# Optimization experiments

Hardware: AMD Instinct MI355X
Metric: run time of the kernel (lower is better)

The kernel has to match this reference:

```python
import jax, jax.numpy as jnp
import numpy as np

T, B, I, H, O = 512, 64, 512, 1024, 512


def setup_inputs() -> dict:
    key = jax.random.key(0)
    ks = jax.random.split(key, 12)
    k = 1.0 / np.sqrt(H)  # torch LSTM/Linear init scale
    u = lambda kk, shape: jax.random.uniform(kk, shape, jnp.float32, -k, k)
    return {
        "x": jax.random.normal(ks[0], (T, B, I), jnp.float32),
        # layer 0 (input -> hidden)
        "W_ih0": u(ks[1], (4 * H, I)),
        "W_hh0": u(ks[2], (4 * H, H)),
        "b_ih0": u(ks[3], (4 * H,)),
        "b_hh0": u(ks[4], (4 * H,)),
        # layer 1 (hidden -> hidden)
        "W_ih1": u(ks[5], (4 * H, H)),
        "W_hh1": u(ks[6], (4 * H, H)),
        "b_ih1": u(ks[7], (4 * H,)),
        "b_hh1": u(ks[8], (4 * H,)),
        # output projection
        "W_out": u(ks[9], (O, H)),
        "b_out": u(ks[10], (O,)),
    }


def _lstm_layer(x_seq, W_ih, W_hh, b_ih, b_hh):
    """x_seq: [T, B, in]; returns hidden sequence [T, B, H].
    PyTorch gate order: i, f, g, o."""
    Hh = W_hh.shape[1]
    Bb = x_seq.shape[1]
    # precompute input contribution for all timesteps (one big GEMM)
    pre = jnp.einsum('tbi,gi->tbg', x_seq, W_ih) + b_ih + b_hh  # [T, B, 4H]

    def step(carry, pre_t):
        h, c = carry
        gates = pre_t + h @ W_hh.T  # [B, 4H]
        i, f, g, o = jnp.split(gates, 4, axis=-1)
        i = jax.nn.sigmoid(i)
        f = jax.nn.sigmoid(f)
        g = jnp.tanh(g)
        o = jax.nn.sigmoid(o)
        c = f * c + i * g
        h = o * jnp.tanh(c)
        return (h, c), h

    h0 = jnp.zeros((Bb, Hh), x_seq.dtype)
    c0 = jnp.zeros((Bb, Hh), x_seq.dtype)
    _, hs = jax.lax.scan(step, (h0, c0), pre)
    return hs  # [T, B, H]


def reference(x, W_ih0, W_hh0, b_ih0, b_hh0, W_ih1, W_hh1, b_ih1, b_hh1, W_out, b_out):
    h1 = _lstm_layer(x, W_ih0, W_hh0, b_ih0, b_hh0)   # [T, B, H]
    h2 = _lstm_layer(h1, W_ih1, W_hh1, b_ih1, b_hh1)  # [T, B, H]
    return jnp.einsum('tbh,oh->tbo', h2, W_out) + b_out  # [T, B, O]
```

## Files before the change

### kernel.cpp

```cpp
#include <hip/hip_runtime.h>
#include <hip/hip_bf16.h>
#include <cstdint>
#include <cstddef>

typedef short bf16x8 __attribute__((ext_vector_type(8)));
typedef float f32x4  __attribute__((ext_vector_type(4)));
typedef __hip_bfloat16 bf16;

#define NT_T 512
#define NB   64
#define NI   512
#define NH   1024
#define NO   512

static constexpr size_t SLOT_E = (size_t)NB * NH + 128;
static constexpr size_t SLOT_B = SLOT_E * 2;

static constexpr size_t OFF_XBF   = 0;
static constexpr size_t SZ_XBF    = (size_t)NT_T * NB * NI * 2;
static constexpr size_t OFF_WSW0  = OFF_XBF + SZ_XBF;
static constexpr size_t SZ_WSW0   = 128ull * 98304;
static constexpr size_t OFF_WSW1  = OFF_WSW0 + SZ_WSW0;
static constexpr size_t SZ_WSW1   = 128ull * 131072;
static constexpr size_t OFF_WOUT  = OFF_WSW1 + SZ_WSW1;
static constexpr size_t SZ_WOUT   = (size_t)NO * NH * 2;
static constexpr size_t OFF_B0    = OFF_WOUT + SZ_WOUT;
static constexpr size_t OFF_B1    = OFF_B0 + 4096 * 4;
static constexpr size_t OFF_H1    = OFF_B1 + 4096 * 4;
static constexpr size_t SZ_H1     = (size_t)NT_T * SLOT_B;
static constexpr size_t OFF_H2    = OFF_H1 + SZ_H1;
static constexpr size_t SZ_H2     = (size_t)NT_T * SLOT_B;
static constexpr size_t OFF_FLG   = OFF_H2 + SZ_H2;
static constexpr size_t SZ_FLG    = 2ull * 128 * 512 * 2;

__device__ __forceinline__ float sigm(float x) {
  return 1.0f / (1.0f + __expf(-x));
}
__device__ __forceinline__ float tanh_fast(float x) {
  x = fminf(15.0f, fmaxf(-15.0f, x));
  const float e = __expf(2.0f * x);
  return (e - 1.0f) / (e + 1.0f);
}

__device__ __forceinline__ void waitf1(const unsigned short* f) {
  while (!__all(__hip_atomic_load(f, __ATOMIC_RELAXED, __HIP_MEMORY_SCOPE_AGENT) != 0))
    __builtin_amdgcn_s_sleep(1);
  asm volatile("" ::: "memory");
}
__device__ __forceinline__ void waitf2(const unsigned short* f0, const unsigned short* f1) {
  while (true) {
    const int a = __hip_atomic_load(f0, __ATOMIC_RELAXED, __HIP_MEMORY_SCOPE_AGENT);
    const int b = __hip_atomic_load(f1, __ATOMIC_RELAXED, __HIP_MEMORY_SCOPE_AGENT);
    if (__all((a != 0) && (b != 0))) break;
    __builtin_amdgcn_s_sleep(1);
  }
  asm volatile("" ::: "memory");
}

template <int N>
__device__ __forceinline__ void load_batch(bf16x8 (&A)[N][2], const bf16* p0, const bf16* p1) {
#pragma unroll
  for (int i = 0; i < N; ++i) {
    A[i][0] = *(const bf16x8*)(p0 + i * 32);
    A[i][1] = *(const bf16x8*)(p1 + i * 32);
  }
}

template <int N, int KSW>
__device__ __forceinline__ void mfma_batch(f32x4 (&acc)[2][2], const bf16x8 (&A)[N][2],
                                           const char* Wlds, int ksbase, int lane) {
#pragma unroll
  for (int i = 0; i < N; ++i) {
#pragma unroll
    for (int nt = 0; nt < 2; ++nt) {
      const bf16x8 b = *(const bf16x8*)(Wlds + ((size_t)(nt * KSW + ksbase + i) * 64 + lane) * 16);
      acc[0][nt] = __builtin_amdgcn_mfma_f32_16x16x32_bf16(A[i][0], b, acc[0][nt], 0, 0, 0);
      acc[1][nt] = __builtin_amdgcn_mfma_f32_16x16x32_bf16(A[i][1], b, acc[1][nt], 0, 0, 0);
    }
  }
}

__global__ void k_convert_x(const float* __restrict__ x, bf16* __restrict__ xbf) {
  const size_t n = (size_t)NT_T * NB * NI;
  for (size_t i = (size_t)blockIdx.x * blockDim.x + threadIdx.x; i < n;
       i += (size_t)gridDim.x * blockDim.x)
    xbf[i] = __float2bfloat16(x[i]);
}

__global__ void k_build_wsw(const float* __restrict__ Wih0, const float* __restrict__ Whh0,
                            const float* __restrict__ Wih1, const float* __restrict__ Whh1,
                            bf16* __restrict__ wsw0, bf16* __restrict__ wsw1) {
  const size_t L0N = 128ull * 2 * 48 * 64 * 8;
  const size_t L1N = 128ull * 2 * 64 * 64 * 8;
  const size_t n = L0N + L1N;
  for (size_t i = (size_t)blockIdx.x * blockDim.x + threadIdx.x; i < n;
       i += (size_t)gridDim.x * blockDim.x) {
    if (i < L0N) {
      size_t idx = i;
      const int j = idx & 7;    idx >>= 3;
      const int lane = idx & 63; idx >>= 6;
      const int ks = (int)(idx % 48); idx /= 48;
      const int nt = idx & 1;
      const int blk = (int)(idx >> 1);
      const int nl = nt * 16 + (lane & 15);
      const int k = ks * 32 + (lane >> 4) * 8 + j;
      const int grow = (nl >> 3) * 1024 + blk * 8 + (nl & 7);
      const float v = (k < 512) ? Wih0[(size_t)grow * 512 + k]
                                : Whh0[(size_t)grow * 1024 + (k - 512)];
      wsw0[i] = __float2bfloat16(v);
    } else {
      size_t idx = i - L0N;
      const size_t o = idx;
      const int j = idx & 7;    idx >>= 3;
      const int lane = idx & 63; idx >>= 6;
      const int ks = (int)(idx % 64); idx /= 64;
      const int nt = idx & 1;
      const int blk = (int)(idx >> 1);
      const int nl = nt * 16 + (lane & 15);
      const int k = ks * 32 + (lane >> 4) * 8 + j;
      const int grow = (nl >> 3) * 1024 + blk * 8 + (nl & 7);
      const float v = (k < 1024) ? Wih1[(size_t)grow * 1024 + k]
                                 : Whh1[(size_t)grow * 1024 + (k - 1024)];
      wsw1[o] = __float2bfloat16(v);
    }
  }
}

__global__ void k_small(const float* __restrict__ Wout,
                        const float* __restrict__ bih0, const float* __restrict__ bhh0,
                        const float* __restrict__ bih1, const float* __restrict__ bhh1,
                        bf16* __restrict__ woutbf, float* __restrict__ bias0,
                        float* __restrict__ bias1, unsigned int* __restrict__ flg) {
  const int i = blockIdx.x * 256 + threadIdx.x;
  if (i < NO * NH) woutbf[i] = __float2bfloat16(Wout[i]);
  if (i < 4096) {
    bias0[i] = bih0[i] + bhh0[i];
    bias1[i] = bih1[i] + bhh1[i];
  }
  if (i < (int)(SZ_FLG / 4)) flg[i] = 0u;
}

__global__ __launch_bounds__(256, 1) void lstm_recur(
    const bf16* __restrict__ xbf, const bf16* __restrict__ wsw0, const bf16* __restrict__ wsw1,
    const float* __restrict__ bias0, const float* __restrict__ bias1,
    bf16* __restrict__ h1hist, bf16* __restrict__ h2hist, unsigned short* __restrict__ flg) {
  __shared__ char Wlds[131072];
  __shared__ float red[64][33];

  const int tid = threadIdx.x;
  const int bid = blockIdx.x;
  const int layer = bid >> 7;
  const int blk = bid & 127;
  const int lane = tid & 63;
  const int wid = tid >> 6;
  const int mh = wid & 1;
  const int kh = wid >> 1;
  const int q = lane >> 4;
  const int ml = lane & 15;
  const int colbase = blk * 8;
  const int row0 = mh * 32 + ml;
  const int row1 = mh * 32 + 16 + ml;

  {
    const char* src = layer ? (const char*)wsw1 + (size_t)blk * 131072
                            : (const char*)wsw0 + (size_t)blk * 98304;
    const int nb = layer ? 131072 : 98304;
    for (int off = tid * 16; off < nb; off += 256 * 16)
      *(uint4*)(Wlds + off) = *(const uint4*)(src + off);
  }

  float biasv[2];
  {
    const float* bs = layer ? bias1 : bias0;
#pragma unroll
    for (int nt = 0; nt < 2; ++nt) {
      const int nl = nt * 16 + ml;
      biasv[nt] = bs[(nl >> 3) * 1024 + colbase + (nl & 7)];
    }
  }
  __syncthreads();

  float cstate[2] = {0.f, 0.f};
  const f32x4 zacc = {0.f, 0.f, 0.f, 0.f};
  const char* WldsC = Wlds;

  const unsigned short* f_l0 = flg;
  const unsigned short* f_l1 = flg + ((size_t)128 << 9);
  unsigned short* fme = flg + (((size_t)layer * 128 + blk) << 9);

  for (int t = 0; t < NT_T; ++t) {
    const bf16* h1prev = h1hist + (size_t)(t - 1) * SLOT_E;
    const bf16* h1cur  = h1hist + (size_t)t * SLOT_E;
    const bf16* h2prev = h2hist + (size_t)(t - 1) * SLOT_E;

    f32x4 acc[2][2];
#pragma unroll
    for (int a1 = 0; a1 < 2; ++a1)
#pragma unroll
      for (int a2 = 0; a2 < 2; ++a2) acc[a1][a2] = zacc;

    if (layer == 0) {
      const bf16* xb = xbf + (size_t)t * NB * NI;
      const int kx = kh * 256 + q * 8;
      bf16x8 Ax[8][2];
      load_batch<8>(Ax, xb + (size_t)row0 * NI + kx, xb + (size_t)row1 * NI + kx);
      if (t > 0) {
        waitf1(f_l0 + (((size_t)(kh * 64 + lane)) << 9) + (t - 1));
        const int khh = kh * 512 + q * 8;
        bf16x8 Ah[16][2];
        load_batch<16>(Ah, h1prev + (size_t)row0 * NH + khh,
                       h1prev + (size_t)row1 * NH + khh);
        __builtin_amdgcn_sched_barrier(0);
        mfma_batch<8, 48>(acc, Ax, WldsC, kh * 8, lane);
        mfma_batch<16, 48>(acc, Ah, WldsC, 16 + kh * 16, lane);
      } else {
        __builtin_amdgcn_sched_barrier(0);
        mfma_batch<8, 48>(acc, Ax, WldsC, kh * 8, lane);
      }
    } else {
      if (kh == 0) {
        waitf2(f_l0 + ((size_t)lane << 9) + t,
               f_l0 + (((size_t)(64 + lane)) << 9) + t);
        bf16x8 Ah[32][2];
        load_batch<32>(Ah, h1cur + (size_t)row0 * NH + q * 8,
                       h1cur + (size_t)row1 * NH + q * 8);
        __builtin_amdgcn_sched_barrier(0);
        mfma_batch<32, 64>(acc, Ah, WldsC, 0, lane);
      } else if (t > 0) {
        waitf2(f_l1 + ((size_t)lane << 9) + (t - 1),
               f_l1 + (((size_t)(64 + lane)) << 9) + (t - 1));
        bf16x8 Ah[32][2];
        load_batch<32>(Ah, h2prev + (size_t)row0 * NH + q * 8,
                       h2prev + (size_t)row1 * NH + q * 8);
        __builtin_amdgcn_sched_barrier(0);
        mfma_batch<32, 64>(acc, Ah, WldsC, 32, lane);
      }
    }

    if (kh == 1) {
#pragma unroll
      for (int mt = 0; mt < 2; ++mt)
#pragma unroll
        for (int nt = 0; nt < 2; ++nt)
#pragma unroll
          for (int r = 0; r < 4; ++r)
            red[mh * 32 + mt * 16 + q * 4 + r][nt * 16 + ml] = acc[mt][nt][r];
    }
    __syncthreads();
    if (kh == 0) {
#pragma unroll
      for (int mt = 0; mt < 2; ++mt)
#pragma unroll
        for (int nt = 0; nt < 2; ++nt)
#pragma unroll
          for (int r = 0; r < 4; ++r) {
            const int mloc = mh * 32 + mt * 16 + q * 4 + r;
            const int nloc = nt * 16 + ml;
            red[mloc][nloc] = acc[mt][nt][r] + red[mloc][nloc] + biasv[nt];
          }
    }
    __syncthreads();

    {
      const int b = tid >> 2;
      const int cc0 = (tid & 3) * 2;
      unsigned short hb[2];
#pragma unroll
      for (int e2 = 0; e2 < 2; ++e2) {
        const int cc = cc0 + e2;
        const float gi = red[b][cc];
        const float gf = red[b][8 + cc];
        const float gg = red[b][16 + cc];
        const float go = red[b][24 + cc];
        const float cn = sigm(gf) * cstate[e2] + sigm(gi) * tanh_fast(gg);
        cstate[e2] = cn;
        const float hv = sigm(go) * tanh_fast(cn);
        hb[e2] = __builtin_bit_cast(unsigned short, __float2bfloat16(hv));
      }
      const unsigned int packed = (unsigned int)hb[0] | ((unsigned int)hb[1] << 16);
      bf16* dstbase = (layer ? h2hist : h1hist) + (size_t)t * SLOT_E + (size_t)b * NH;
      __hip_atomic_store((unsigned int*)(dstbase + colbase + cc0), packed,
                         __ATOMIC_RELAXED, __HIP_MEMORY_SCOPE_AGENT);
    }

    __syncthreads();
    if (tid == 0)
      __hip_atomic_store(fme + t, (unsigned short)1,
                         __ATOMIC_RELAXED, __HIP_MEMORY_SCOPE_AGENT);
  }
}

__global__ __launch_bounds__(256) void gemm_out(
    const bf16* __restrict__ A, const bf16* __restrict__ B,
    const float* __restrict__ bout, float* __restrict__ out) {
  __shared__ char As[8192];
  __shared__ char Bs[8192];
  const int tid = threadIdx.x;
  const int lane = tid & 63;
  const int wid = tid >> 6;
  const int wm = wid >> 1;
  const int wn = wid & 1;
  const size_t Mbase = (size_t)blockIdx.y * 128;
  const int Nbase = blockIdx.x * 128;

  const f32x4 zacc = {0.f, 0.f, 0.f, 0.f};
  f32x4 acc[4][4];
#pragma unroll
  for (int i = 0; i < 4; ++i)
#pragma unroll
    for (int j = 0; j < 4; ++j) acc[i][j] = zacc;

  for (int kc = 0; kc < 32; ++kc) {
    const int kb = kc * 32;
#pragma unroll
    for (int e = 0; e < 2; ++e) {
      const int id = e * 256 + tid;
      const int r = id >> 2;
      const int c8 = (id & 3) * 8;
      const int dst = ((r >> 4) * 64 + (c8 >> 3) * 16 + (r & 15)) * 16;
      const size_t m = Mbase + r;
      const bf16* arow = A + (m >> 6) * SLOT_E + (size_t)(m & 63) * NH;
      *(uint4*)(As + dst) = *(const uint4*)(arow + kb + c8);
      *(uint4*)(Bs + dst) = *(const uint4*)(B + (size_t)(Nbase + r) * NH + kb + c8);
    }
    __syncthreads();
    bf16x8 af[4], bfr[4];
#pragma unroll
    for (int i = 0; i < 4; ++i) {
      af[i]  = *(const bf16x8*)(As + ((wm * 4 + i) * 64 + lane) * 16);
      bfr[i] = *(const bf16x8*)(Bs + ((wn * 4 + i) * 64 + lane) * 16);
    }
#pragma unroll
    for (int i = 0; i < 4; ++i)
#pragma unroll
      for (int j = 0; j < 4; ++j)
        acc[i][j] = __builtin_amdgcn_mfma_f32_16x16x32_bf16(af[i], bfr[j], acc[i][j], 0, 0, 0);
    __syncthreads();
  }
  const int qq = lane >> 4, ml = lane & 15;
#pragma unroll
  for (int i = 0; i < 4; ++i)
#pragma unroll
    for (int j = 0; j < 4; ++j)
#pragma unroll
      for (int r = 0; r < 4; ++r) {
        const size_t m = Mbase + wm * 64 + i * 16 + qq * 4 + r;
        const int n = Nbase + wn * 64 + j * 16 + ml;
        out[m * NO + n] = acc[i][j][r] + bout[n];
      }
}

extern "C" void kernel_launch(void* const* d_in, const int* in_sizes, int n_in,
                              void* d_out, int out_size, void* d_ws, size_t ws_size,
                              hipStream_t stream) {
  (void)in_sizes; (void)n_in; (void)out_size; (void)ws_size;
  const float* x    = (const float*)d_in[0];
  const float* Wih0 = (const float*)d_in[1];
  const float* Whh0 = (const float*)d_in[2];
  const float* bih0 = (const float*)d_in[3];
  const float* bhh0 = (const float*)d_in[4];
  const float* Wih1 = (const float*)d_in[5];
  const float* Whh1 = (const float*)d_in[6];
  const float* bih1 = (const float*)d_in[7];
  const float* bhh1 = (const float*)d_in[8];
  const float* Wout = (const float*)d_in[9];
  const float* bout = (const float*)d_in[10];
  float* out = (float*)d_out;
  char* ws = (char*)d_ws;

  bf16*  xbf    = (bf16*)(ws + OFF_XBF);
  bf16*  wsw0   = (bf16*)(ws + OFF_WSW0);
  bf16*  wsw1   = (bf16*)(ws + OFF_WSW1);
  bf16*  woutbf = (bf16*)(ws + OFF_WOUT);
  float* bias0  = (float*)(ws + OFF_B0);
  float* bias1  = (float*)(ws + OFF_B1);
  bf16*  h1hist = (bf16*)(ws + OFF_H1);
  bf16*  h2hist = (bf16*)(ws + OFF_H2);
  unsigned short* flg = (unsigned short*)(ws + OFF_FLG);

  k_convert_x<<<8192, 256, 0, stream>>>(x, xbf);
  k_build_wsw<<<14336, 256, 0, stream>>>(Wih0, Whh0, Wih1, Whh1, wsw0, wsw1);
  k_small<<<2048, 256, 0, stream>>>(Wout, bih0, bhh0, bih1, bhh1, woutbf, bias0, bias1,
                                    (unsigned int*)flg);
  lstm_recur<<<256, 256, 0, stream>>>(xbf, wsw0, wsw1, bias0, bias1, h1hist, h2hist, flg);
  gemm_out<<<dim3(4, 256), 256, 0, stream>>>(h2hist, woutbf, bout, out);
}
```

Measured before the change: 5.488 ms.

## Split recurrent LSTM K-reduction across eight waves per block

Doubles the persistent recurrent kernel's block size from 256 to 512 threads. Each wave now handles half of its previous K-slice, which halves per-wave global loads and MFMA chains. Partial sums from three extra slots are reduced through a larger shared buffer. The aim is to shorten the per-timestep critical path by using more wavefronts per CU. The cost is more LDS traffic, a four-way reduction, and half the threads sitting idle during the gate nonlinearity phase.

```diff
diff --git a/kernel.cpp b/kernel.cpp
--- a/kernel.cpp
+++ b/kernel.cpp
@@ -45,15 +45,6 @@
 __device__ __forceinline__ void waitf1(const unsigned short* f) {
   while (!__all(__hip_atomic_load(f, __ATOMIC_RELAXED, __HIP_MEMORY_SCOPE_AGENT) != 0))
     __builtin_amdgcn_s_sleep(1);
-  asm volatile("" ::: "memory");
-}
-__device__ __forceinline__ void waitf2(const unsigned short* f0, const unsigned short* f1) {
-  while (true) {
-    const int a = __hip_atomic_load(f0, __ATOMIC_RELAXED, __HIP_MEMORY_SCOPE_AGENT);
-    const int b = __hip_atomic_load(f1, __ATOMIC_RELAXED, __HIP_MEMORY_SCOPE_AGENT);
-    if (__all((a != 0) && (b != 0))) break;
-    __builtin_amdgcn_s_sleep(1);
-  }
   asm volatile("" ::: "memory");
 }
 
@@ -140,12 +131,12 @@
   if (i < (int)(SZ_FLG / 4)) flg[i] = 0u;
 }
 
-__global__ __launch_bounds__(256, 1) void lstm_recur(
+__global__ __launch_bounds__(512, 1) void lstm_recur(
     const bf16* __restrict__ xbf, const bf16* __restrict__ wsw0, const bf16* __restrict__ wsw1,
     const float* __restrict__ bias0, const float* __restrict__ bias1,
     bf16* __restrict__ h1hist, bf16* __restrict__ h2hist, unsigned short* __restrict__ flg) {
   __shared__ char Wlds[131072];
-  __shared__ float red[64][33];
+  __shared__ float red[3][64][33];
 
   const int tid = threadIdx.x;
   const int bid = blockIdx.x;
@@ -154,18 +145,20 @@
   const int lane = tid & 63;
   const int wid = tid >> 6;
   const int mh = wid & 1;
-  const int kh = wid >> 1;
+  const int kh = (wid >> 1) & 1;
+  const int hf = wid >> 2;
   const int q = lane >> 4;
   const int ml = lane & 15;
   const int colbase = blk * 8;
   const int row0 = mh * 32 + ml;
   const int row1 = mh * 32 + 16 + ml;
+  const int slot = kh * 2 + hf - 1;
 
   {
     const char* src = layer ? (const char*)wsw1 + (size_t)blk * 131072
                             : (const char*)wsw0 + (size_t)blk * 98304;
     const int nb = layer ? 131072 : 98304;
-    for (int off = tid * 16; off < nb; off += 256 * 16)
+    for (int off = tid * 16; off < nb; off += 512 * 16)
       *(uint4*)(Wlds + off) = *(const uint4*)(src + off);
   }
 
@@ -201,53 +194,53 @@
 
     if (layer == 0) {
       const bf16* xb = xbf + (size_t)t * NB * NI;
-      const int kx = kh * 256 + q * 8;
-      bf16x8 Ax[8][2];
-      load_batch<8>(Ax, xb + (size_t)row0 * NI + kx, xb + (size_t)row1 * NI + kx);
+      const int kx = kh * 256 + hf * 128 + q * 8;
+      bf16x8 Ax[4][2];
+      load_batch<4>(Ax, xb + (size_t)row0 * NI + kx, xb + (size_t)row1 * NI + kx);
       if (t > 0) {
-        waitf1(f_l0 + (((size_t)(kh * 64 + lane)) << 9) + (t - 1));
-        const int khh = kh * 512 + q * 8;
-        bf16x8 Ah[16][2];
-        load_batch<16>(Ah, h1prev + (size_t)row0 * NH + khh,
-                       h1prev + (size_t)row1 * NH + khh);
+        waitf1(f_l0 + (((size_t)(kh * 64 + hf * 32 + (lane & 31))) << 9) + (t - 1));
+        const int khh = kh * 512 + hf * 256 + q * 8;
+        bf16x8 Ah[8][2];
+        load_batch<8>(Ah, h1prev + (size_t)row0 * NH + khh,
+                      h1prev + (size_t)row1 * NH + khh);
         __builtin_amdgcn_sched_barrier(0);
-        mfma_batch<8, 48>(acc, Ax, WldsC, kh * 8, lane);
-        mfma_batch<16, 48>(acc, Ah, WldsC, 16 + kh * 16, lane);
+        mfma_batch<4, 48>(acc, Ax, WldsC, kh * 8 + hf * 4, lane);
+        mfma_batch<8, 48>(acc, Ah, WldsC, 16 + kh * 16 + hf * 8, lane);
       } else {
         __builtin_amdgcn_sched_barrier(0);
-        mfma_batch<8, 48>(acc, Ax, WldsC, kh * 8, lane);
+        mfma_batch<4, 48>(acc, Ax, WldsC, kh * 8 + hf * 4, lane);
       }
     } else {
       if (kh == 0) {
-        waitf2(f_l0 + ((size_t)lane << 9) + t,
-               f_l0 + (((size_t)(64 + lane)) << 9) + t);
-        bf16x8 Ah[32][2];
-        load_batch<32>(Ah, h1cur + (size_t)row0 * NH + q * 8,
-                       h1cur + (size_t)row1 * NH + q * 8);
+        waitf1(f_l0 + (((size_t)(hf * 64 + lane)) << 9) + t);
+        const bf16* hp0 = h1cur + (size_t)row0 * NH + hf * 512 + q * 8;
+        const bf16* hp1 = h1cur + (size_t)row1 * NH + hf * 512 + q * 8;
+        bf16x8 Ah[16][2];
+        load_batch<16>(Ah, hp0, hp1);
         __builtin_amdgcn_sched_barrier(0);
-        mfma_batch<32, 64>(acc, Ah, WldsC, 0, lane);
+        mfma_batch<16, 64>(acc, Ah, WldsC, hf * 16, lane);
       } else if (t > 0) {
-        waitf2(f_l1 + ((size_t)lane << 9) + (t - 1),
-               f_l1 + (((size_t)(64 + lane)) << 9) + (t - 1));
-        bf16x8 Ah[32][2];
-        load_batch<32>(Ah, h2prev + (size_t)row0 * NH + q * 8,
-                       h2prev + (size_t)row1 * NH + q * 8);
+        waitf1(f_l1 + (((size_t)(hf * 64 + lane)) << 9) + (t - 1));
+        const bf16* hp0 = h2prev + (size_t)row0 * NH + hf * 512 + q * 8;
+        const bf16* hp1 = h2prev + (size_t)row1 * NH + hf * 512 + q * 8;
+        bf16x8 Ah[16][2];
+        load_batch<16>(Ah, hp0, hp1);
         __builtin_amdgcn_sched_barrier(0);
-        mfma_batch<32, 64>(acc, Ah, WldsC, 32, lane);
+        mfma_batch<16, 64>(acc, Ah, WldsC, 32 + hf * 16, lane);
       }
     }
 
-    if (kh == 1) {
+    if (slot >= 0) {
 #pragma unroll
       for (int mt = 0; mt < 2; ++mt)
 #pragma unroll
         for (int nt = 0; nt < 2; ++nt)
 #pragma unroll
           for (int r = 0; r < 4; ++r)
-            red[mh * 32 + mt * 16 + q * 4 + r][nt * 16 + ml] = acc[mt][nt][r];
-    }
-    __syncthreads();
-    if (kh == 0) {
+            red[slot][mh * 32 + mt * 16 + q * 4 + r][nt * 16 + ml] = acc[mt][nt][r];
+    }
+    __syncthreads();
+    if (slot < 0) {
 #pragma unroll
       for (int mt = 0; mt < 2; ++mt)
 #pragma unroll
@@ -256,22 +249,23 @@
           for (int r = 0; r < 4; ++r) {
             const int mloc = mh * 32 + mt * 16 + q * 4 + r;
             const int nloc = nt * 16 + ml;
-            red[mloc][nloc] = acc[mt][nt][r] + red[mloc][nloc] + biasv[nt];
+            red[0][mloc][nloc] = acc[mt][nt][r] + red[0][mloc][nloc] +
+                                 red[1][mloc][nloc] + red[2][mloc][nloc] + biasv[nt];
           }
     }
     __syncthreads();
 
-    {
+    if (tid < 256) {
       const int b = tid >> 2;
       const int cc0 = (tid & 3) * 2;
       unsigned short hb[2];
 #pragma unroll
       for (int e2 = 0; e2 < 2; ++e2) {
         const int cc = cc0 + e2;
-        const float gi = red[b][cc];
-        const float gf = red[b][8 + cc];
-        const float gg = red[b][16 + cc];
-        const float go = red[b][24 + cc];
+        const float gi = red[0][b][cc];
+        const float gf = red[0][b][8 + cc];
+        const float gg = red[0][b][16 + cc];
+        const float go = red[0][b][24 + cc];
         const float cn = sigm(gf) * cstate[e2] + sigm(gi) * tanh_fast(gg);
         cstate[e2] = cn;
         const float hv = sigm(go) * tanh_fast(cn);
@@ -382,6 +376,6 @@
   k_build_wsw<<<14336, 256, 0, stream>>>(Wih0, Whh0, Wih1, Whh1, wsw0, wsw1);
   k_small<<<2048, 256, 0, stream>>>(Wout, bih0, bhh0, bih1, bhh1, woutbf, bias0, bias1,
                                     (unsigned int*)flg);
-  lstm_recur<<<256, 256, 0, stream>>>(xbf, wsw0, wsw1, bias0, bias1, h1hist, h2hist, flg);
+  lstm_recur<<<256, 512, 0, stream>>>(xbf, wsw0, wsw1, bias0, bias1, h1hist, h2hist, flg);
   gemm_out<<<dim3(4, 256), 256, 0, stream>>>(h2hist, woutbf, bout, out);
 }
```

Result: faster. 5.030 ms (-8.3%).
